# Performance work log

Measured on AMD Instinct MI355X. Metric: run time of the kernel, lower is better.

## Reference

```python
import jax, jax.numpy as jnp
import numpy as np

NUM_EXPERTS = 8
TOP_K = 2
D_MODEL = 1024
D_FF = 4096
B, S = 2, 2048


def setup_inputs() -> dict:
    key = jax.random.key(0)
    k1, k2, k3, k4 = jax.random.split(key, 4)
    scale_in = 1.0 / np.sqrt(D_MODEL)
    scale_ff = 1.0 / np.sqrt(D_FF)
    return {
        "hidden_states": jax.random.normal(k1, (B, S, D_MODEL), dtype=jnp.float32),
        "gate_w": jax.random.normal(k2, (D_MODEL, NUM_EXPERTS), dtype=jnp.float32) * scale_in,
        "w1": jax.random.normal(k3, (NUM_EXPERTS, D_MODEL, D_FF), dtype=jnp.float32) * scale_in,
        "w2": jax.random.normal(k4, (NUM_EXPERTS, D_FF, D_MODEL), dtype=jnp.float32) * scale_ff,
    }


def reference(hidden_states, gate_w, w1, w2):
    b, s, d = hidden_states.shape
    x = hidden_states.reshape(-1, d)                      # [T, d]
    gate_logits = x @ gate_w                              # [T, E]
    top_vals, top_idx = jax.lax.top_k(gate_logits, TOP_K)  # [T, K]
    # softmax over selected expert logits in fp32, cast back
    top_w = jax.nn.softmax(top_vals.astype(jnp.float32), axis=1).astype(x.dtype)
    # per-token per-expert combine weight: sum_k w[t,k] * (sel[t,k]==e)
    combine = jnp.einsum("tke,tk->te", jax.nn.one_hot(top_idx, NUM_EXPERTS, dtype=x.dtype), top_w)  # [T, E]
    # naive dense MoE: every expert over all tokens (matches torch loop)
    h = jax.nn.relu(jnp.einsum("td,edf->etf", x, w1))     # [E, T, d_ff]
    expert_out = jnp.einsum("etf,efd->etd", h, w2)        # [E, T, d]
    final = jnp.einsum("etd,te->td", expert_out, combine)  # [T, d]
    return final.reshape(b, s, d)
```

## Files before the change

kernel.cpp:

```cpp
#include <hip/hip_runtime.h>
#include <hip/hip_bf16.h>
#include <stdint.h>


#define T_TOK 4096
#define DM 1024
#define DF 4096
#define NE 8
#define BM 128
#define BN 128
#define BK 64
#define MAX_TILES 72
#define PAIR_CAP 9216

typedef __bf16 bf16x8 __attribute__((ext_vector_type(8)));
typedef float f32x4 __attribute__((ext_vector_type(4)));
typedef unsigned short ushort_t;

__device__ __forceinline__ ushort_t f2bf(float f) {
  uint32_t u = __float_as_uint(f);
  u += 0x7FFFu + ((u >> 16) & 1u);
  return (ushort_t)(u >> 16);
}

#define WT_OFF  0ull
#define XB_OFF  67108864ull
#define H_OFF   75497472ull
#define PO_OFF  159383552ull
#define RT_OFF  201326592ull
#define RO_COUNTS   0
#define RO_OFFSETS  32
#define RO_CURSORS  64
#define RO_NTILES   96
#define RO_TILE_E   128
#define RO_TILE_S   448
#define RO_TILE_R   768
#define RO_PTOK     1088
#define RO_PW       37952
#define RO_TOPI     74816
#define RO_TOPW     107584
#define RO_PIDX     140352
#define RT_BYTES    173120ull
#define WS_NEEDED   (RT_OFF + RT_BYTES)

__device__ __forceinline__ int xcd_work(int b, int live) {
  int k = b & 7, j = b >> 3;
  int q = live >> 3, r = live & 7;
  int cnt = q + (k < r ? 1 : 0);
  if (j >= cnt) return -1;
  int start = k * q + (k < r ? k : r);
  return start + j;
}

__global__ void gate_kernel(const float* __restrict__ x, const float* __restrict__ gw,
                            int* __restrict__ counts, int* __restrict__ topi,
                            float* __restrict__ topw, ushort_t* __restrict__ xb) {
  int wave = threadIdx.x >> 6;
  int lane = threadIdx.x & 63;
  int t = blockIdx.x * 4 + wave;
  const float* xr = x + (size_t)t * DM;
  ushort_t* xbr = xb + (size_t)t * DM;
  float acc[NE];
#pragma unroll
  for (int e = 0; e < NE; ++e) acc[e] = 0.f;
  for (int d = lane; d < DM; d += 64) {
    float xv = xr[d];
    xbr[d] = f2bf(xv);
    const float* g = gw + (size_t)d * NE;
#pragma unroll
    for (int e = 0; e < NE; ++e) acc[e] += xv * g[e];
  }
#pragma unroll
  for (int off = 32; off > 0; off >>= 1) {
#pragma unroll
    for (int e = 0; e < NE; ++e) acc[e] += __shfl_xor(acc[e], off, 64);
  }
  if (lane == 0) {
    int i0 = 0; float v0 = acc[0];
#pragma unroll
    for (int e = 1; e < NE; ++e) if (acc[e] > v0) { v0 = acc[e]; i0 = e; }
    int i1 = -1; float v1 = -1e30f;
#pragma unroll
    for (int e = 0; e < NE; ++e) if (e != i0 && acc[e] > v1) { v1 = acc[e]; i1 = e; }
    float e1 = expf(v1 - v0);
    float w0 = 1.f / (1.f + e1);
    float w1 = e1 / (1.f + e1);
    topi[t * 2] = i0; topi[t * 2 + 1] = i1;
    topw[t * 2] = w0; topw[t * 2 + 1] = w1;
    atomicAdd(&counts[i0], 1);
    atomicAdd(&counts[i1], 1);
  }
}

__global__ void scan_kernel(const int* __restrict__ counts, int* __restrict__ offsets,
                            int* __restrict__ cursors, int* __restrict__ n_tiles,
                            int* __restrict__ tile_e, int* __restrict__ tile_s,
                            int* __restrict__ tile_r) {
  if (threadIdx.x == 0) {
    int off = 0, nt = 0;
    for (int e = 0; e < NE; ++e) {
      offsets[e] = off;
      cursors[e] = 0;
      int c = counts[e];
      for (int m0 = 0; m0 < c; m0 += BM) {
        tile_e[nt] = e;
        tile_s[nt] = off + m0;
        tile_r[nt] = (c - m0 < BM) ? (c - m0) : BM;
        ++nt;
      }
      off += ((c + BM - 1) / BM) * BM;
    }
    *n_tiles = nt;
  }
}

__global__ void scatter_kernel(const int* __restrict__ topi, const float* __restrict__ topw,
                               const int* __restrict__ offsets, int* __restrict__ cursors,
                               int* __restrict__ ptok, float* __restrict__ pw,
                               int* __restrict__ pidx) {
  int t = blockIdx.x * 256 + threadIdx.x;
  if (t >= T_TOK) return;
#pragma unroll
  for (int k = 0; k < 2; ++k) {
    int e = topi[t * 2 + k];
    int pos = atomicAdd(&cursors[e], 1);
    int p = offsets[e] + pos;
    ptok[p] = t;
    pw[p] = topw[t * 2 + k];
    pidx[t * 2 + k] = p;
  }
}

__global__ void transpose_convert(const float* __restrict__ src, ushort_t* __restrict__ dst,
                                  int R, int C) {
  __shared__ ushort_t tile[64][136];
  int e = blockIdx.z;
  src += (size_t)e * R * C;
  dst += (size_t)e * R * C;
  int c0 = blockIdx.x * 64, r0 = blockIdx.y * 128;
  int tr = threadIdx.x >> 4;
  int tc = (threadIdx.x & 15) << 2;
#pragma unroll
  for (int i = 0; i < 8; ++i) {
    int r = i * 16 + tr;
    float4 v = *(const float4*)&src[(size_t)(r0 + r) * C + c0 + tc];
    tile[tc + 0][r] = f2bf(v.x);
    tile[tc + 1][r] = f2bf(v.y);
    tile[tc + 2][r] = f2bf(v.z);
    tile[tc + 3][r] = f2bf(v.w);
  }
  __syncthreads();
  int cr = threadIdx.x >> 5;
  int rg = (threadIdx.x & 31) << 2;
#pragma unroll
  for (int j = 0; j < 8; ++j) {
    int c = j * 8 + cr;
    ushort4 o = { tile[c][rg], tile[c][rg + 1], tile[c][rg + 2], tile[c][rg + 3] };
    *(ushort4*)&dst[(size_t)(c0 + c) * R + r0 + rg] = o;
  }
}


#define GLD(srcp, dstp)                                                        \
  __builtin_amdgcn_global_load_lds(                                            \
      (const __attribute__((address_space(1))) void*)(srcp),                   \
      (__attribute__((address_space(3))) void*)(dstp), 16, 0, 0)

__device__ __forceinline__ void gemm_core(
    ushort_t* As, ushort_t* Bs,
    const ushort_t* const (&a_sp)[4], const ushort_t* const (&b_sp)[4],
    int NT, int wid, int lane, f32x4 (&acc)[4][4]) {
  int fr = lane & 15, ch = lane >> 4, sw = lane & 7;
  int k0s = (ch ^ sw) * 8;
  int k1s = ((ch + 4) ^ sw) * 8;
  int m_off = (wid >> 1) * 64, n_off = (wid & 1) * 64;
  int abase = (m_off + fr) * 64;
  int bbase = (n_off + fr) * 64;

  for (int t = 0; t < NT; ++t) {
    int k0 = t * BK;
#pragma unroll
    for (int j = 0; j < 4; ++j) {
      GLD(a_sp[j] + k0, As + (wid * 4 + j) * 512);
      GLD(b_sp[j] + k0, Bs + (wid * 4 + j) * 512);
    }
    asm volatile("s_waitcnt vmcnt(0)" ::: "memory");
    __syncthreads();

#pragma unroll
    for (int kx = 0; kx < 2; ++kx) {
      int ks = kx ? k1s : k0s;
      bf16x8 af[4], bf[4];
#pragma unroll
      for (int mi = 0; mi < 4; ++mi) af[mi] = *(const bf16x8*)&As[abase + mi * 1024 + ks];
#pragma unroll
      for (int ni = 0; ni < 4; ++ni) bf[ni] = *(const bf16x8*)&Bs[bbase + ni * 1024 + ks];
#pragma unroll
      for (int mi = 0; mi < 4; ++mi)
#pragma unroll
        for (int ni = 0; ni < 4; ++ni)
          acc[mi][ni] = __builtin_amdgcn_mfma_f32_16x16x32_bf16(af[mi], bf[ni], acc[mi][ni], 0, 0, 0);
    }
    __syncthreads();
  }
}

__global__ __launch_bounds__(256, 3) void gemm1_kernel(
    const ushort_t* __restrict__ xb, const ushort_t* __restrict__ w1t,
    ushort_t* __restrict__ h,
    const int* __restrict__ n_tiles, const int* __restrict__ tile_e,
    const int* __restrict__ tile_s, const int* __restrict__ tile_r,
    const int* __restrict__ ptok) {
  int work = xcd_work(blockIdx.x, *n_tiles * (DF / BN));
  if (work < 0) return;
  int tile = work >> 5;
  int n0 = (work & 31) * BN;
  int e = tile_e[tile], p0 = tile_s[tile], rows = tile_r[tile];

  __shared__ ushort_t As[BM * BK];
  __shared__ ushort_t Bs[BN * BK];
  int tid = threadIdx.x, wid = tid >> 6, lane = tid & 63;
  int lr = lane >> 3;
  int swc = (lane & 7) ^ (lr & 7);

  const ushort_t* a_sp[4];
  const ushort_t* b_sp[4];
#pragma unroll
  for (int j = 0; j < 4; ++j) {
    int r = wid * 32 + j * 8 + lr;
    int tok = (r < rows) ? ptok[p0 + r] : 0;
    a_sp[j] = xb + (size_t)tok * DM + swc * 8;
    b_sp[j] = w1t + ((size_t)e * DF + n0 + r) * DM + swc * 8;
  }

  f32x4 acc[4][4] = {};
  gemm_core(As, Bs, a_sp, b_sp, DM / BK, wid, lane, acc);

  int m_off = (wid >> 1) * 64, n_off = (wid & 1) * 64;
  int col = lane & 15, rq = (lane >> 4) * 4;
#pragma unroll
  for (int mi = 0; mi < 4; ++mi)
#pragma unroll
    for (int r = 0; r < 4; ++r) {
      int m = m_off + mi * 16 + rq + r;
      bool valid = m < rows;
      size_t rowoff = (size_t)(p0 + m) * DF + n0 + n_off;
#pragma unroll
      for (int ni = 0; ni < 4; ++ni) {
        float v = acc[mi][ni][r];
        v = valid ? (v > 0.f ? v : 0.f) : 0.f;
        h[rowoff + ni * 16 + col] = f2bf(v);
      }
    }
}

__global__ __launch_bounds__(256, 3) void gemm2_kernel(
    const ushort_t* __restrict__ h, const ushort_t* __restrict__ w2t,
    float* __restrict__ po,
    const int* __restrict__ n_tiles, const int* __restrict__ tile_e,
    const int* __restrict__ tile_s, const int* __restrict__ tile_r,
    const float* __restrict__ pw) {
  int work = xcd_work(blockIdx.x, *n_tiles * (DM / BN));
  if (work < 0) return;
  int tile = work >> 3;
  int n0 = (work & 7) * BN;
  int e = tile_e[tile], p0 = tile_s[tile], rows = tile_r[tile];

  __shared__ ushort_t As[BM * BK];
  __shared__ ushort_t Bs[BN * BK];
  int tid = threadIdx.x, wid = tid >> 6, lane = tid & 63;
  int lr = lane >> 3;
  int swc = (lane & 7) ^ (lr & 7);

  const ushort_t* a_sp[4];
  const ushort_t* b_sp[4];
#pragma unroll
  for (int j = 0; j < 4; ++j) {
    int r = wid * 32 + j * 8 + lr;
    a_sp[j] = h + (size_t)(p0 + r) * DF + swc * 8;
    b_sp[j] = w2t + ((size_t)e * DM + n0 + r) * DF + swc * 8;
  }

  f32x4 acc[4][4] = {};
  gemm_core(As, Bs, a_sp, b_sp, DF / BK, wid, lane, acc);

  int m_off = (wid >> 1) * 64, n_off = (wid & 1) * 64;
  int col = lane & 15, rq = (lane >> 4) * 4;
#pragma unroll
  for (int mi = 0; mi < 4; ++mi)
#pragma unroll
    for (int r = 0; r < 4; ++r) {
      int m = m_off + mi * 16 + rq + r;
      if (m < rows) {
        int p = p0 + m;
        float w = pw[p];
        size_t o = (size_t)p * DM + n0 + n_off;
#pragma unroll
        for (int ni = 0; ni < 4; ++ni)
          po[o + ni * 16 + col] = w * acc[mi][ni][r];
      }
    }
}

__global__ void combine_kernel(const float* __restrict__ po, const int* __restrict__ pidx,
                               float* __restrict__ out) {
  int idx = blockIdx.x * 256 + threadIdx.x;
  int t = idx >> 8;
  int d4 = (idx & 255) << 2;
  int pa = pidx[t * 2], pb = pidx[t * 2 + 1];
  float4 a = *(const float4*)&po[(size_t)pa * DM + d4];
  float4 b = *(const float4*)&po[(size_t)pb * DM + d4];
  float4 o = { a.x + b.x, a.y + b.y, a.z + b.z, a.w + b.w };
  *(float4*)&out[(size_t)t * DM + d4] = o;
}

extern "C" void kernel_launch(void* const* d_in, const int* in_sizes, int n_in,
                              void* d_out, int out_size, void* d_ws, size_t ws_size,
                              hipStream_t stream) {
  const float* x  = (const float*)d_in[0];
  const float* gw = (const float*)d_in[1];
  const float* w1 = (const float*)d_in[2];
  const float* w2 = (const float*)d_in[3];
  float* out = (float*)d_out;
  char* ws = (char*)d_ws;
  if (ws_size < WS_NEEDED) return;

  ushort_t* wt  = (ushort_t*)(ws + WT_OFF);
  ushort_t* xb  = (ushort_t*)(ws + XB_OFF);
  ushort_t* h   = (ushort_t*)(ws + H_OFF);
  float*    po  = (float*)(ws + PO_OFF);
  char* rt = ws + RT_OFF;
  int*   counts  = (int*)(rt + RO_COUNTS);
  int*   offsets = (int*)(rt + RO_OFFSETS);
  int*   cursors = (int*)(rt + RO_CURSORS);
  int*   n_tiles = (int*)(rt + RO_NTILES);
  int*   tile_e  = (int*)(rt + RO_TILE_E);
  int*   tile_s  = (int*)(rt + RO_TILE_S);
  int*   tile_r  = (int*)(rt + RO_TILE_R);
  int*   ptok    = (int*)(rt + RO_PTOK);
  float* pw      = (float*)(rt + RO_PW);
  int*   topi    = (int*)(rt + RO_TOPI);
  float* topw    = (float*)(rt + RO_TOPW);
  int*   pidx    = (int*)(rt + RO_PIDX);

  hipMemsetAsync(rt, 0, 128, stream);

  hipLaunchKernelGGL(gate_kernel, dim3(T_TOK / 4), dim3(256), 0, stream,
                     x, gw, counts, topi, topw, xb);
  hipLaunchKernelGGL(scan_kernel, dim3(1), dim3(64), 0, stream,
                     counts, offsets, cursors, n_tiles, tile_e, tile_s, tile_r);
  hipLaunchKernelGGL(scatter_kernel, dim3(T_TOK / 256), dim3(256), 0, stream,
                     topi, topw, offsets, cursors, ptok, pw, pidx);
  hipLaunchKernelGGL(transpose_convert, dim3(DF / 64, DM / 128, NE), dim3(256), 0, stream,
                     w1, wt, DM, DF);
  hipLaunchKernelGGL(gemm1_kernel, dim3(MAX_TILES * (DF / BN)), dim3(256), 0, stream,
                     xb, wt, h, n_tiles, tile_e, tile_s, tile_r, ptok);
  hipLaunchKernelGGL(transpose_convert, dim3(DM / 64, DF / 128, NE), dim3(256), 0, stream,
                     w2, wt, DF, DM);
  hipLaunchKernelGGL(gemm2_kernel, dim3(MAX_TILES * (DM / BN)), dim3(256), 0, stream,
                     h, wt, po, n_tiles, tile_e, tile_s, tile_r, pw);
  hipLaunchKernelGGL(combine_kernel, dim3((T_TOK * DM / 4) / 256), dim3(256), 0, stream,
                     po, pidx, out);
}
```

Before: 421.9 us.

## Split-K gemm2 in two halves with bf16 partials and four-way combine

Gemm2 now splits the 4096-deep reduction into two halves, doubling the number of work items so more CUs stay busy on the small per-expert tiles. Each half writes weighted partial outputs as bf16 into separate buffers, and the combine kernel sums four bf16 partials per output element (two experts times two K halves). Launch bounds for both GEMMs also go from 3 to 4 waves per SIMD. Storing partials in bf16 halves the partial-output traffic but adds rounding error, and the higher occupancy target may force register spills.

```diff
diff --git a/kernel.cpp b/kernel.cpp
--- a/kernel.cpp
+++ b/kernel.cpp
@@ -22,6 +22,8 @@
   u += 0x7FFFu + ((u >> 16) & 1u);
   return (ushort_t)(u >> 16);
 }
+__device__ __forceinline__ float bfl(uint32_t u) { return __uint_as_float(u << 16); }
+__device__ __forceinline__ float bfh(uint32_t u) { return __uint_as_float(u & 0xFFFF0000u); }
 
 #define WT_OFF  0ull
 #define XB_OFF  67108864ull
@@ -205,7 +207,7 @@
   }
 }
 
-__global__ __launch_bounds__(256, 3) void gemm1_kernel(
+__global__ __launch_bounds__(256, 4) void gemm1_kernel(
     const ushort_t* __restrict__ xb, const ushort_t* __restrict__ w1t,
     ushort_t* __restrict__ h,
     const int* __restrict__ n_tiles, const int* __restrict__ tile_e,
@@ -254,16 +256,19 @@
     }
 }
 
-__global__ __launch_bounds__(256, 3) void gemm2_kernel(
+__global__ __launch_bounds__(256, 4) void gemm2_kernel(
     const ushort_t* __restrict__ h, const ushort_t* __restrict__ w2t,
-    float* __restrict__ po,
+    ushort_t* __restrict__ po,
     const int* __restrict__ n_tiles, const int* __restrict__ tile_e,
     const int* __restrict__ tile_s, const int* __restrict__ tile_r,
     const float* __restrict__ pw) {
-  int work = xcd_work(blockIdx.x, *n_tiles * (DM / BN));
+  int work = xcd_work(blockIdx.x, *n_tiles * (DM / BN) * 2);
   if (work < 0) return;
-  int tile = work >> 3;
-  int n0 = (work & 7) * BN;
+  int tile = work >> 4;
+  int sub = work & 15;
+  int n0 = (sub >> 1) * BN;
+  int kh = sub & 1;
+  int kof = kh * (DF / 2);
   int e = tile_e[tile], p0 = tile_s[tile], rows = tile_r[tile];
 
   __shared__ ushort_t As[BM * BK];
@@ -277,13 +282,14 @@
 #pragma unroll
   for (int j = 0; j < 4; ++j) {
     int r = wid * 32 + j * 8 + lr;
-    a_sp[j] = h + (size_t)(p0 + r) * DF + swc * 8;
-    b_sp[j] = w2t + ((size_t)e * DM + n0 + r) * DF + swc * 8;
+    a_sp[j] = h + (size_t)(p0 + r) * DF + kof + swc * 8;
+    b_sp[j] = w2t + ((size_t)e * DM + n0 + r) * DF + kof + swc * 8;
   }
 
   f32x4 acc[4][4] = {};
-  gemm_core(As, Bs, a_sp, b_sp, DF / BK, wid, lane, acc);
-
+  gemm_core(As, Bs, a_sp, b_sp, DF / (2 * BK), wid, lane, acc);
+
+  ushort_t* pod = po + (size_t)kh * PAIR_CAP * DM;
   int m_off = (wid >> 1) * 64, n_off = (wid & 1) * 64;
   int col = lane & 15, rq = (lane >> 4) * 4;
 #pragma unroll
@@ -297,21 +303,38 @@
         size_t o = (size_t)p * DM + n0 + n_off;
 #pragma unroll
         for (int ni = 0; ni < 4; ++ni)
-          po[o + ni * 16 + col] = w * acc[mi][ni][r];
+          pod[o + ni * 16 + col] = f2bf(w * acc[mi][ni][r]);
       }
     }
 }
 
-__global__ void combine_kernel(const float* __restrict__ po, const int* __restrict__ pidx,
+__global__ void combine_kernel(const ushort_t* __restrict__ po, const int* __restrict__ pidx,
                                float* __restrict__ out) {
   int idx = blockIdx.x * 256 + threadIdx.x;
-  int t = idx >> 8;
-  int d4 = (idx & 255) << 2;
+  int t = idx >> 7;
+  int d8 = (idx & 127) << 3;
   int pa = pidx[t * 2], pb = pidx[t * 2 + 1];
-  float4 a = *(const float4*)&po[(size_t)pa * DM + d4];
-  float4 b = *(const float4*)&po[(size_t)pb * DM + d4];
-  float4 o = { a.x + b.x, a.y + b.y, a.z + b.z, a.w + b.w };
-  *(float4*)&out[(size_t)t * DM + d4] = o;
+  const size_t HS = (size_t)PAIR_CAP * DM;
+  size_t oa = (size_t)pa * DM + d8, ob = (size_t)pb * DM + d8;
+  uint4 va0 = *(const uint4*)&po[oa];
+  uint4 vb0 = *(const uint4*)&po[ob];
+  uint4 va1 = *(const uint4*)&po[HS + oa];
+  uint4 vb1 = *(const uint4*)&po[HS + ob];
+  const uint32_t* A0 = (const uint32_t*)&va0;
+  const uint32_t* B0 = (const uint32_t*)&vb0;
+  const uint32_t* A1 = (const uint32_t*)&va1;
+  const uint32_t* B1 = (const uint32_t*)&vb1;
+  float r[8];
+#pragma unroll
+  for (int w = 0; w < 4; ++w) {
+    r[2 * w]     = bfl(A0[w]) + bfl(B0[w]) + bfl(A1[w]) + bfl(B1[w]);
+    r[2 * w + 1] = bfh(A0[w]) + bfh(B0[w]) + bfh(A1[w]) + bfh(B1[w]);
+  }
+  float4 o0 = { r[0], r[1], r[2], r[3] };
+  float4 o1 = { r[4], r[5], r[6], r[7] };
+  size_t ob2 = (size_t)t * DM + d8;
+  *(float4*)&out[ob2] = o0;
+  *(float4*)&out[ob2 + 4] = o1;
 }
 
 extern "C" void kernel_launch(void* const* d_in, const int* in_sizes, int n_in,
@@ -328,7 +351,7 @@
   ushort_t* wt  = (ushort_t*)(ws + WT_OFF);
   ushort_t* xb  = (ushort_t*)(ws + XB_OFF);
   ushort_t* h   = (ushort_t*)(ws + H_OFF);
-  float*    po  = (float*)(ws + PO_OFF);
+  ushort_t* po  = (ushort_t*)(ws + PO_OFF);
   char* rt = ws + RT_OFF;
   int*   counts  = (int*)(rt + RO_COUNTS);
   int*   offsets = (int*)(rt + RO_OFFSETS);
@@ -357,8 +380,8 @@
                      xb, wt, h, n_tiles, tile_e, tile_s, tile_r, ptok);
   hipLaunchKernelGGL(transpose_convert, dim3(DM / 64, DF / 128, NE), dim3(256), 0, stream,
                      w2, wt, DF, DM);
-  hipLaunchKernelGGL(gemm2_kernel, dim3(MAX_TILES * (DM / BN)), dim3(256), 0, stream,
+  hipLaunchKernelGGL(gemm2_kernel, dim3(MAX_TILES * (DM / BN) * 2), dim3(256), 0, stream,
                      h, wt, po, n_tiles, tile_e, tile_s, tile_r, pw);
-  hipLaunchKernelGGL(combine_kernel, dim3((T_TOK * DM / 4) / 256), dim3(256), 0, stream,
+  hipLaunchKernelGGL(combine_kernel, dim3((T_TOK * DM / 8) / 256), dim3(256), 0, stream,
                      po, pidx, out);
 }
```

Result: no change. 419.6 us (-0.5%).

## Fuse MoE combine into gemm2 via atomic adds and vectorize gate loads

Applied to the files above, without the earlier changes.

Removes the separate per-pair output buffer and combine kernel. gemm2 now scatter-adds weighted results straight into the zeroed output with float atomics, indexed by token, which adds a memset of the output. The gate kernel switches to float4 loads and vector bf16 stores, and the GEMM launch bounds go from 3 to 4 waves per SIMD. Atomic adds of two contributions per element make the summation order nondeterministic and may cost more than plain stores, and the tighter launch bound may force register spills.

```diff
diff --git a/kernel.cpp b/kernel.cpp
--- a/kernel.cpp
+++ b/kernel.cpp
@@ -26,7 +26,6 @@
 #define WT_OFF  0ull
 #define XB_OFF  67108864ull
 #define H_OFF   75497472ull
-#define PO_OFF  159383552ull
 #define RT_OFF  201326592ull
 #define RO_COUNTS   0
 #define RO_OFFSETS  32
@@ -39,8 +38,7 @@
 #define RO_PW       37952
 #define RO_TOPI     74816
 #define RO_TOPW     107584
-#define RO_PIDX     140352
-#define RT_BYTES    173120ull
+#define RT_BYTES    140352ull
 #define WS_NEEDED   (RT_OFF + RT_BYTES)
 
 __device__ __forceinline__ int xcd_work(int b, int live) {
@@ -63,12 +61,16 @@
   float acc[NE];
 #pragma unroll
   for (int e = 0; e < NE; ++e) acc[e] = 0.f;
-  for (int d = lane; d < DM; d += 64) {
-    float xv = xr[d];
-    xbr[d] = f2bf(xv);
-    const float* g = gw + (size_t)d * NE;
-#pragma unroll
-    for (int e = 0; e < NE; ++e) acc[e] += xv * g[e];
+#pragma unroll
+  for (int it = 0; it < DM / 256; ++it) {
+    int d0 = (it * 64 + lane) * 4;
+    float4 v = *(const float4*)&xr[d0];
+    ushort4 o = { f2bf(v.x), f2bf(v.y), f2bf(v.z), f2bf(v.w) };
+    *(ushort4*)&xbr[d0] = o;
+    const float* g0 = gw + (size_t)d0 * NE;
+#pragma unroll
+    for (int e = 0; e < NE; ++e)
+      acc[e] += v.x * g0[e] + v.y * g0[NE + e] + v.z * g0[2 * NE + e] + v.w * g0[3 * NE + e];
   }
 #pragma unroll
   for (int off = 32; off > 0; off >>= 1) {
@@ -116,8 +118,7 @@
 
 __global__ void scatter_kernel(const int* __restrict__ topi, const float* __restrict__ topw,
                                const int* __restrict__ offsets, int* __restrict__ cursors,
-                               int* __restrict__ ptok, float* __restrict__ pw,
-                               int* __restrict__ pidx) {
+                               int* __restrict__ ptok, float* __restrict__ pw) {
   int t = blockIdx.x * 256 + threadIdx.x;
   if (t >= T_TOK) return;
 #pragma unroll
@@ -127,7 +128,6 @@
     int p = offsets[e] + pos;
     ptok[p] = t;
     pw[p] = topw[t * 2 + k];
-    pidx[t * 2 + k] = p;
   }
 }
 
@@ -205,7 +205,7 @@
   }
 }
 
-__global__ __launch_bounds__(256, 3) void gemm1_kernel(
+__global__ __launch_bounds__(256, 4) void gemm1_kernel(
     const ushort_t* __restrict__ xb, const ushort_t* __restrict__ w1t,
     ushort_t* __restrict__ h,
     const int* __restrict__ n_tiles, const int* __restrict__ tile_e,
@@ -254,12 +254,12 @@
     }
 }
 
-__global__ __launch_bounds__(256, 3) void gemm2_kernel(
+__global__ __launch_bounds__(256, 4) void gemm2_kernel(
     const ushort_t* __restrict__ h, const ushort_t* __restrict__ w2t,
-    float* __restrict__ po,
+    float* __restrict__ out,
     const int* __restrict__ n_tiles, const int* __restrict__ tile_e,
     const int* __restrict__ tile_s, const int* __restrict__ tile_r,
-    const float* __restrict__ pw) {
+    const int* __restrict__ ptok, const float* __restrict__ pw) {
   int work = xcd_work(blockIdx.x, *n_tiles * (DM / BN));
   if (work < 0) return;
   int tile = work >> 3;
@@ -293,25 +293,14 @@
       int m = m_off + mi * 16 + rq + r;
       if (m < rows) {
         int p = p0 + m;
+        int tok = ptok[p];
         float w = pw[p];
-        size_t o = (size_t)p * DM + n0 + n_off;
+        size_t o = (size_t)tok * DM + n0 + n_off;
 #pragma unroll
         for (int ni = 0; ni < 4; ++ni)
-          po[o + ni * 16 + col] = w * acc[mi][ni][r];
+          atomicAdd(&out[o + ni * 16 + col], w * acc[mi][ni][r]);
       }
     }
-}
-
-__global__ void combine_kernel(const float* __restrict__ po, const int* __restrict__ pidx,
-                               float* __restrict__ out) {
-  int idx = blockIdx.x * 256 + threadIdx.x;
-  int t = idx >> 8;
-  int d4 = (idx & 255) << 2;
-  int pa = pidx[t * 2], pb = pidx[t * 2 + 1];
-  float4 a = *(const float4*)&po[(size_t)pa * DM + d4];
-  float4 b = *(const float4*)&po[(size_t)pb * DM + d4];
-  float4 o = { a.x + b.x, a.y + b.y, a.z + b.z, a.w + b.w };
-  *(float4*)&out[(size_t)t * DM + d4] = o;
 }
 
 extern "C" void kernel_launch(void* const* d_in, const int* in_sizes, int n_in,
@@ -328,7 +317,6 @@
   ushort_t* wt  = (ushort_t*)(ws + WT_OFF);
   ushort_t* xb  = (ushort_t*)(ws + XB_OFF);
   ushort_t* h   = (ushort_t*)(ws + H_OFF);
-  float*    po  = (float*)(ws + PO_OFF);
   char* rt = ws + RT_OFF;
   int*   counts  = (int*)(rt + RO_COUNTS);
   int*   offsets = (int*)(rt + RO_OFFSETS);
@@ -341,16 +329,16 @@
   float* pw      = (float*)(rt + RO_PW);
   int*   topi    = (int*)(rt + RO_TOPI);
   float* topw    = (float*)(rt + RO_TOPW);
-  int*   pidx    = (int*)(rt + RO_PIDX);
 
   hipMemsetAsync(rt, 0, 128, stream);
+  hipMemsetAsync(out, 0, (size_t)T_TOK * DM * sizeof(float), stream);
 
   hipLaunchKernelGGL(gate_kernel, dim3(T_TOK / 4), dim3(256), 0, stream,
                      x, gw, counts, topi, topw, xb);
   hipLaunchKernelGGL(scan_kernel, dim3(1), dim3(64), 0, stream,
                      counts, offsets, cursors, n_tiles, tile_e, tile_s, tile_r);
   hipLaunchKernelGGL(scatter_kernel, dim3(T_TOK / 256), dim3(256), 0, stream,
-                     topi, topw, offsets, cursors, ptok, pw, pidx);
+                     topi, topw, offsets, cursors, ptok, pw);
   hipLaunchKernelGGL(transpose_convert, dim3(DF / 64, DM / 128, NE), dim3(256), 0, stream,
                      w1, wt, DM, DF);
   hipLaunchKernelGGL(gemm1_kernel, dim3(MAX_TILES * (DF / BN)), dim3(256), 0, stream,
@@ -358,7 +346,5 @@
   hipLaunchKernelGGL(transpose_convert, dim3(DM / 64, DF / 128, NE), dim3(256), 0, stream,
                      w2, wt, DF, DM);
   hipLaunchKernelGGL(gemm2_kernel, dim3(MAX_TILES * (DM / BN)), dim3(256), 0, stream,
-                     h, wt, po, n_tiles, tile_e, tile_s, tile_r, pw);
-  hipLaunchKernelGGL(combine_kernel, dim3((T_TOK * DM / 4) / 256), dim3(256), 0, stream,
-                     po, pidx, out);
-}
+                     h, wt, out, n_tiles, tile_e, tile_s, tile_r, ptok, pw);
+}
```

After: 422.1 us. About the same (+0.1%).
